# Optimization experiments

Measured on AMD Instinct MI355X. Metric: run time of the kernel, lower is better.

## Reference

```python
import jax, jax.numpy as jnp
import numpy as np

X_MIN, X_MAX = -3.0, 3.0
EPS = 1e-08


def setup_inputs() -> dict:
    key = jax.random.key(0)
    k1, k2, k3 = jax.random.split(key, 3)
    B, D_in, D_out, K = 8192, 512, 128, 16
    x = jax.random.normal(k1, (B, D_in), dtype=jnp.float32)
    # trunc_normal_(std=0.02) approximated by scaled normal
    weights = jax.random.normal(k2, (D_out, D_in, K), dtype=jnp.float32) * 0.02
    # xavier_uniform for skip
    limit = float(np.sqrt(6.0 / (D_in + D_out)))
    skip_w = jax.random.uniform(k3, (D_out, D_in), dtype=jnp.float32,
                                minval=-limit, maxval=limit)
    bias = jnp.zeros((D_out,), dtype=jnp.float32)
    return {"x": x, "weights": weights, "skip_w": skip_w, "bias": bias}


def reference(x, weights, skip_w, bias):
    # x: (B, D_in); weights: (D_out, D_in, K); skip_w: (D_out, D_in); bias: (D_out,)
    K = weights.shape[-1]
    t = jnp.clip((x - X_MIN) / (X_MAX - X_MIN + EPS), 0.0, 1.0)
    pos = t * (K - 1)
    idx0 = jnp.floor(pos).astype(jnp.int32)
    idx1 = jnp.minimum(idx0 + 1, K - 1)
    frac = jnp.clip(pos - idx0.astype(pos.dtype), 0.0, 1.0)
    # Hat-basis coefficients per (b, i): avoids materializing (B, D_out, D_in)
    oh0 = jax.nn.one_hot(idx0, K, dtype=x.dtype)  # (B, D_in, K)
    oh1 = jax.nn.one_hot(idx1, K, dtype=x.dtype)
    c = oh0 * (1.0 - frac)[..., None] + oh1 * frac[..., None]  # (B, D_in, K)
    # y[b,o] = sum_i (1-frac)*w[o,i,idx0] + frac*w[o,i,idx1]
    y = jnp.einsum('bik,oik->bo', c, weights)
    y = y + bias + x @ skip_w.T
    return y
```

## Files before the change

kernel.cpp:

```cpp
#include <hip/hip_runtime.h>

typedef _Float16 half8 __attribute__((ext_vector_type(8)));
typedef _Float16 h16 __attribute__((ext_vector_type(16)));
typedef float f32x4 __attribute__((ext_vector_type(4)));

#define DIN 512
#define DOUT 128
#define BTOT 8192
#define NCHUNK 68
#define NSPL 8
#define BM 128
#define CHUNK_BYTES 32768
#define CBASE 32768
#define LDS_BYTES 65536

__device__ static inline void llds16(const char* g, char* l) {
  __builtin_amdgcn_global_load_lds(
      (const __attribute__((address_space(1))) unsigned int*)g,
      (__attribute__((address_space(3))) unsigned int*)l, 16, 0, 0);
}

__device__ static inline unsigned short f2h(float x) {
  _Float16 h = (_Float16)x;
  return __builtin_bit_cast(unsigned short, h);
}

__global__ __launch_bounds__(256) void build_wpp(const float* __restrict__ w,
                                                 const float* __restrict__ sk,
                                                 unsigned short* __restrict__ wpp) {
  const int gid = blockIdx.x * 256 + threadIdx.x;
  const int g = gid >> 11;
  const int rem = gid & 2047;
  const int p = rem >> 7;
  const int o = rem & 127;
  const int kglob = g * 128 + p * 8;
  const float* src = (kglob < 8192) ? (w + (size_t)o * 8192 + kglob)
                                    : (sk + (size_t)o * 512 + (kglob - 8192));
  const float4 v0 = ((const float4*)src)[0];
  const float4 v1 = ((const float4*)src)[1];
  uint4 pk;
  pk.x = f2h(v0.x) | ((unsigned)f2h(v0.y) << 16);
  pk.y = f2h(v0.z) | ((unsigned)f2h(v0.w) << 16);
  pk.z = f2h(v1.x) | ((unsigned)f2h(v1.y) << 16);
  pk.w = f2h(v1.z) | ((unsigned)f2h(v1.w) << 16);
  ((uint4*)wpp)[gid] = pk;
}

__global__ __launch_bounds__(256) void xpose(const float* __restrict__ x,
                                             _Float16* __restrict__ xt) {
  __shared__ _Float16 t[32][33];
  const int c0 = blockIdx.x * 32;
  const int r0 = blockIdx.y * 32;
  const int tx = threadIdx.x & 31, ty = threadIdx.x >> 5;
#pragma unroll
  for (int j = 0; j < 32; j += 8)
    t[ty + j][tx] = (_Float16)x[(size_t)(r0 + ty + j) * DIN + c0 + tx];
  __syncthreads();
#pragma unroll
  for (int j = 0; j < 32; j += 8)
    xt[(size_t)(c0 + ty + j) * BTOT + r0 + tx] = t[tx][ty + j];
}

__global__ __launch_bounds__(256, 2) void kan_mfma(
    const float* __restrict__ x, const _Float16* __restrict__ xt,
    const unsigned short* __restrict__ wpp, const float* __restrict__ bias,
    float* __restrict__ out) {
  __shared__ __align__(16) char smem[LDS_BYTES];
  const int tid = threadIdx.x;
  const int bt = blockIdx.x >> 3;
  const int sp = blockIdx.x & 7;
  const int b0 = bt * BM;
  const int wid = tid >> 6, lane = tid & 63;
  const int lr = lane & 15, lq = lane >> 4;
  const int wm = wid & 1, wn = wid >> 1;

  const h16 iota16 = {(_Float16)0, (_Float16)1, (_Float16)2, (_Float16)3,
                      (_Float16)4, (_Float16)5, (_Float16)6, (_Float16)7,
                      (_Float16)8, (_Float16)9, (_Float16)10, (_Float16)11,
                      (_Float16)12, (_Float16)13, (_Float16)14, (_Float16)15};
  const h16 one16 = {(_Float16)1, (_Float16)1, (_Float16)1, (_Float16)1,
                     (_Float16)1, (_Float16)1, (_Float16)1, (_Float16)1,
                     (_Float16)1, (_Float16)1, (_Float16)1, (_Float16)1,
                     (_Float16)1, (_Float16)1, (_Float16)1, (_Float16)1};
  const h16 zero16 = {};

  f32x4 acc[4][4] = {};

  for (int c = 0; c < 9; ++c) {
    int g;
    bool skipc;
    if (c < 8) { g = sp + c * 8; skipc = false; }
    else { if (sp >= 4) break; g = 64 + sp; skipc = true; }

    __syncthreads();

    {
      const char* gsrc = (const char*)wpp + (size_t)g * CHUNK_BYTES + wid * 8192 + lane * 16;
      char* ldst = smem + wid * 8192;
#pragma unroll
      for (int it = 0; it < 8; ++it)
        llds16(gsrc + it * 1024, ldst + it * 1024);
    }

    if (!skipc) {
      const int ib = g * 8;
#pragma unroll
      for (int hh = 0; hh < 2; ++hh) {
        const int il = wid * 2 + hh;
#pragma unroll
        for (int rh = 0; rh < 2; ++rh) {
          const int r = lane + rh * 64;
          const float xv = (float)xt[(size_t)(ib + il) * BTOT + b0 + r];
          float t = fminf(fmaxf((xv + 3.0f) * (1.0f / 6.0f), 0.0f), 1.0f);
          const float pos = t * 15.0f;
          const _Float16 ph = (_Float16)pos;
          h16 pv;
#pragma unroll
          for (int q = 0; q < 16; ++q) pv[q] = ph;
          h16 d = __builtin_elementwise_abs(pv - iota16);
          h16 cc = __builtin_elementwise_max(one16 - d, zero16);
          char* base = smem + CBASE + (2 * il) * 2048 + r * 16;
          *(uint4*)base = ((const uint4*)&cc)[0];
          *(uint4*)(base + 2048) = ((const uint4*)&cc)[1];
        }
      }
    } else {
      const int ioff = (g - 64) * 128;
#pragma unroll
      for (int pp = 0; pp < 4; ++pp) {
        const int p = wid * 4 + pp;
#pragma unroll
        for (int rh = 0; rh < 2; ++rh) {
          const int r = lane + rh * 64;
          const float* src = x + (size_t)(b0 + r) * DIN + ioff + p * 8;
          const float4 v0 = ((const float4*)src)[0];
          const float4 v1 = ((const float4*)src)[1];
          uint4 pk;
          pk.x = f2h(v0.x) | ((unsigned)f2h(v0.y) << 16);
          pk.y = f2h(v0.z) | ((unsigned)f2h(v0.w) << 16);
          pk.z = f2h(v1.x) | ((unsigned)f2h(v1.y) << 16);
          pk.w = f2h(v1.z) | ((unsigned)f2h(v1.w) << 16);
          *(uint4*)(smem + CBASE + p * 2048 + r * 16) = pk;
        }
      }
    }
    __syncthreads();

#pragma unroll
    for (int ks = 0; ks < 4; ++ks) {
      const int slab = (ks * 4 + lq) * 2048 + lr * 16;
      half8 af[4], bf[4];
#pragma unroll
      for (int mt = 0; mt < 4; ++mt)
        af[mt] = *(const half8*)(smem + CBASE + slab + (wm * 64 + mt * 16) * 16);
#pragma unroll
      for (int nt = 0; nt < 4; ++nt)
        bf[nt] = *(const half8*)(smem + slab + (wn * 64 + nt * 16) * 16);
#pragma unroll
      for (int mt = 0; mt < 4; ++mt)
#pragma unroll
        for (int nt = 0; nt < 4; ++nt)
          acc[mt][nt] = __builtin_amdgcn_mfma_f32_16x16x32_f16(af[mt], bf[nt], acc[mt][nt], 0, 0, 0);
    }
  }

#pragma unroll
  for (int nt = 0; nt < 4; ++nt) {
    const int col = wn * 64 + nt * 16 + lr;
    const float bv = (sp == 0) ? bias[col] : 0.0f;
#pragma unroll
    for (int mt = 0; mt < 4; ++mt) {
      const int row0 = b0 + wm * 64 + mt * 16 + lq * 4;
#pragma unroll
      for (int r = 0; r < 4; ++r)
        atomicAdd(out + (size_t)(row0 + r) * DOUT + col, acc[mt][nt][r] + bv);
    }
  }
}

__global__ void kan_naive(const float* __restrict__ x, const float* __restrict__ w,
                          const float* __restrict__ skw, const float* __restrict__ bias,
                          float* __restrict__ out) {
  const int b = blockIdx.x;
  const int o = threadIdx.x;
  float acc = bias[o];
  for (int i = 0; i < DIN; ++i) {
    float xv = x[(size_t)b * DIN + i];
    float t = fminf(fmaxf((xv + 3.0f) * (1.0f / 6.0f), 0.0f), 1.0f);
    float p = t * 15.0f;
    float fi = floorf(p);
    int i0 = (int)fi;
    int i1 = (i0 < 15) ? i0 + 1 : 15;
    float f = p - fi;
    const float* wr = &w[((size_t)o * DIN + i) * 16];
    acc += (1.0f - f) * wr[i0] + f * wr[i1] + xv * skw[(size_t)o * DIN + i];
  }
  out[(size_t)b * DOUT + o] = acc;
}

extern "C" void kernel_launch(void* const* d_in, const int* in_sizes, int n_in,
                              void* d_out, int out_size, void* d_ws, size_t ws_size,
                              hipStream_t stream) {
  const float* x    = (const float*)d_in[0];
  const float* w    = (const float*)d_in[1];
  const float* skw  = (const float*)d_in[2];
  const float* bias = (const float*)d_in[3];
  float* out = (float*)d_out;

  const size_t xt_bytes = (size_t)DIN * BTOT * sizeof(_Float16);
  const size_t wpp_bytes = (size_t)NCHUNK * CHUNK_BYTES;
  if (ws_size < xt_bytes + wpp_bytes) {
    kan_naive<<<BTOT, DOUT, 0, stream>>>(x, w, skw, bias, out);
    return;
  }

  _Float16* xt = (_Float16*)d_ws;
  unsigned short* wpp = (unsigned short*)((char*)d_ws + xt_bytes);

  (void)hipMemsetAsync(d_out, 0, (size_t)out_size * sizeof(float), stream);
  build_wpp<<<NCHUNK * 2048 / 256, 256, 0, stream>>>(w, skw, wpp);
  xpose<<<dim3(DIN / 32, BTOT / 32), 256, 0, stream>>>(x, xt);
  kan_mfma<<<(BTOT / BM) * NSPL, 256, 0, stream>>>(x, xt, wpp, bias, out);
}
```

Baseline: 122.5 us.

## Read weight fragments from global memory directly and double the K-split

Weight B-fragments are now loaded directly from global/L2 into registers, so they are no longer staged into LDS with global_load_lds. This halves LDS per block, which allows a launch bound of 4 blocks per SM. The K-split goes from 8 to 16 so each block handles 4-5 chunks instead of 8-9, giving more blocks and more parallelism. The trade-offs are uncoalesced-ish global loads in the MFMA loop with no LDS reuse, and twice as many atomicAdds onto the output.

```diff
diff --git a/kernel.cpp b/kernel.cpp
--- a/kernel.cpp
+++ b/kernel.cpp
@@ -8,17 +8,10 @@
 #define DOUT 128
 #define BTOT 8192
 #define NCHUNK 68
-#define NSPL 8
+#define NSPL 16
 #define BM 128
 #define CHUNK_BYTES 32768
-#define CBASE 32768
-#define LDS_BYTES 65536
-
-__device__ static inline void llds16(const char* g, char* l) {
-  __builtin_amdgcn_global_load_lds(
-      (const __attribute__((address_space(1))) unsigned int*)g,
-      (__attribute__((address_space(3))) unsigned int*)l, 16, 0, 0);
-}
+#define LDS_BYTES 32768
 
 __device__ static inline unsigned short f2h(float x) {
   _Float16 h = (_Float16)x;
@@ -61,14 +54,14 @@
     xt[(size_t)(c0 + ty + j) * BTOT + r0 + tx] = t[tx][ty + j];
 }
 
-__global__ __launch_bounds__(256, 2) void kan_mfma(
+__global__ __launch_bounds__(256, 4) void kan_mfma(
     const float* __restrict__ x, const _Float16* __restrict__ xt,
     const unsigned short* __restrict__ wpp, const float* __restrict__ bias,
     float* __restrict__ out) {
   __shared__ __align__(16) char smem[LDS_BYTES];
   const int tid = threadIdx.x;
-  const int bt = blockIdx.x >> 3;
-  const int sp = blockIdx.x & 7;
+  const int bt = blockIdx.x >> 4;
+  const int sp = blockIdx.x & 15;
   const int b0 = bt * BM;
   const int wid = tid >> 6, lane = tid & 63;
   const int lr = lane & 15, lq = lane >> 4;
@@ -85,22 +78,13 @@
   const h16 zero16 = {};
 
   f32x4 acc[4][4] = {};
-
-  for (int c = 0; c < 9; ++c) {
-    int g;
-    bool skipc;
-    if (c < 8) { g = sp + c * 8; skipc = false; }
-    else { if (sp >= 4) break; g = 64 + sp; skipc = true; }
-
-    __syncthreads();
-
-    {
-      const char* gsrc = (const char*)wpp + (size_t)g * CHUNK_BYTES + wid * 8192 + lane * 16;
-      char* ldst = smem + wid * 8192;
-#pragma unroll
-      for (int it = 0; it < 8; ++it)
-        llds16(gsrc + it * 1024, ldst + it * 1024);
-    }
+  const int nch = (sp < 4) ? 5 : 4;
+
+  for (int j = 0; j < nch; ++j) {
+    const int g = (j < 4) ? (sp + j * 16) : (64 + sp);
+    const bool skipc = (j == 4);
+
+    if (j > 0) __syncthreads();
 
     if (!skipc) {
       const int ib = g * 8;
@@ -112,14 +96,13 @@
           const int r = lane + rh * 64;
           const float xv = (float)xt[(size_t)(ib + il) * BTOT + b0 + r];
           float t = fminf(fmaxf((xv + 3.0f) * (1.0f / 6.0f), 0.0f), 1.0f);
-          const float pos = t * 15.0f;
-          const _Float16 ph = (_Float16)pos;
+          const _Float16 ph = (_Float16)(t * 15.0f);
           h16 pv;
 #pragma unroll
           for (int q = 0; q < 16; ++q) pv[q] = ph;
           h16 d = __builtin_elementwise_abs(pv - iota16);
           h16 cc = __builtin_elementwise_max(one16 - d, zero16);
-          char* base = smem + CBASE + (2 * il) * 2048 + r * 16;
+          char* base = smem + (2 * il) * 2048 + r * 16;
           *(uint4*)base = ((const uint4*)&cc)[0];
           *(uint4*)(base + 2048) = ((const uint4*)&cc)[1];
         }
@@ -140,22 +123,24 @@
           pk.y = f2h(v0.z) | ((unsigned)f2h(v0.w) << 16);
           pk.z = f2h(v1.x) | ((unsigned)f2h(v1.y) << 16);
           pk.w = f2h(v1.z) | ((unsigned)f2h(v1.w) << 16);
-          *(uint4*)(smem + CBASE + p * 2048 + r * 16) = pk;
+          *(uint4*)(smem + p * 2048 + r * 16) = pk;
         }
       }
     }
     __syncthreads();
 
+    const char* wchunk = (const char*)wpp + (size_t)g * CHUNK_BYTES
+                       + (size_t)lq * 2048 + (size_t)(wn * 64 + lr) * 16;
 #pragma unroll
     for (int ks = 0; ks < 4; ++ks) {
       const int slab = (ks * 4 + lq) * 2048 + lr * 16;
       half8 af[4], bf[4];
 #pragma unroll
+      for (int nt = 0; nt < 4; ++nt)
+        bf[nt] = *(const half8*)(wchunk + ks * 8192 + nt * 256);
+#pragma unroll
       for (int mt = 0; mt < 4; ++mt)
-        af[mt] = *(const half8*)(smem + CBASE + slab + (wm * 64 + mt * 16) * 16);
-#pragma unroll
-      for (int nt = 0; nt < 4; ++nt)
-        bf[nt] = *(const half8*)(smem + slab + (wn * 64 + nt * 16) * 16);
+        af[mt] = *(const half8*)(smem + slab + (wm * 64 + mt * 16) * 16);
 #pragma unroll
       for (int mt = 0; mt < 4; ++mt)
 #pragma unroll
```

Measured after the change: 143.3 us. 1.17x slower.

## Generate hat coefficients in registers and switch to 32x32 MFMA with 17-way split

Applied to the files above, without the earlier changes.

Replaces the LDS-staged coefficient tile with hat-basis coefficients computed directly in registers, laid out as MFMA A fragments for 32x32x16 f16 instructions. The x transpose kernel becomes a plain row-major fp16 cast, and the skip-path A operands are read straight from global memory. The split-K factor goes from 8 to 17 (4 chunks per block), and halving LDS use allows 3 blocks per CU. In exchange there is more per-lane VALU work per MFMA, strided global reads of A, and more atomic adds into the output.

```diff
diff --git a/kernel.cpp b/kernel.cpp
--- a/kernel.cpp
+++ b/kernel.cpp
@@ -1,18 +1,16 @@
 #include <hip/hip_runtime.h>
 
 typedef _Float16 half8 __attribute__((ext_vector_type(8)));
-typedef _Float16 h16 __attribute__((ext_vector_type(16)));
-typedef float f32x4 __attribute__((ext_vector_type(4)));
+typedef float f32x16 __attribute__((ext_vector_type(16)));
 
 #define DIN 512
 #define DOUT 128
 #define BTOT 8192
 #define NCHUNK 68
-#define NSPL 8
+#define NSPL 17
 #define BM 128
 #define CHUNK_BYTES 32768
-#define CBASE 32768
-#define LDS_BYTES 65536
+#define LDS_BYTES 32768
 
 __device__ static inline void llds16(const char* g, char* l) {
   __builtin_amdgcn_global_load_lds(
@@ -46,54 +44,56 @@
   ((uint4*)wpp)[gid] = pk;
 }
 
-__global__ __launch_bounds__(256) void xpose(const float* __restrict__ x,
-                                             _Float16* __restrict__ xt) {
-  __shared__ _Float16 t[32][33];
-  const int c0 = blockIdx.x * 32;
-  const int r0 = blockIdx.y * 32;
-  const int tx = threadIdx.x & 31, ty = threadIdx.x >> 5;
-#pragma unroll
-  for (int j = 0; j < 32; j += 8)
-    t[ty + j][tx] = (_Float16)x[(size_t)(r0 + ty + j) * DIN + c0 + tx];
-  __syncthreads();
-#pragma unroll
-  for (int j = 0; j < 32; j += 8)
-    xt[(size_t)(c0 + ty + j) * BTOT + r0 + tx] = t[tx][ty + j];
-}
-
-__global__ __launch_bounds__(256, 2) void kan_mfma(
-    const float* __restrict__ x, const _Float16* __restrict__ xt,
-    const unsigned short* __restrict__ wpp, const float* __restrict__ bias,
-    float* __restrict__ out) {
+__global__ __launch_bounds__(256) void xcast(const float* __restrict__ x,
+                                             _Float16* __restrict__ xh) {
+  const int n = (blockIdx.x * 256 + threadIdx.x) * 4;
+  const float4 v = *(const float4*)(x + n);
+  unsigned lo = f2h(v.x) | ((unsigned)f2h(v.y) << 16);
+  unsigned hi = f2h(v.z) | ((unsigned)f2h(v.w) << 16);
+  *(uint2*)(xh + n) = make_uint2(lo, hi);
+}
+
+__global__ __launch_bounds__(256, 3) void kan_mfma(
+    const _Float16* __restrict__ xh, const unsigned short* __restrict__ wpp,
+    const float* __restrict__ bias, float* __restrict__ out) {
   __shared__ __align__(16) char smem[LDS_BYTES];
   const int tid = threadIdx.x;
-  const int bt = blockIdx.x >> 3;
-  const int sp = blockIdx.x & 7;
+  const unsigned u = blockIdx.x;
+  const int bt = u & 63;
+  const int sp = u >> 6;
   const int b0 = bt * BM;
   const int wid = tid >> 6, lane = tid & 63;
-  const int lr = lane & 15, lq = lane >> 4;
+  const int l5 = lane >> 5, l31 = lane & 31;
   const int wm = wid & 1, wn = wid >> 1;
 
-  const h16 iota16 = {(_Float16)0, (_Float16)1, (_Float16)2, (_Float16)3,
-                      (_Float16)4, (_Float16)5, (_Float16)6, (_Float16)7,
-                      (_Float16)8, (_Float16)9, (_Float16)10, (_Float16)11,
-                      (_Float16)12, (_Float16)13, (_Float16)14, (_Float16)15};
-  const h16 one16 = {(_Float16)1, (_Float16)1, (_Float16)1, (_Float16)1,
-                     (_Float16)1, (_Float16)1, (_Float16)1, (_Float16)1,
-                     (_Float16)1, (_Float16)1, (_Float16)1, (_Float16)1,
-                     (_Float16)1, (_Float16)1, (_Float16)1, (_Float16)1};
-  const h16 zero16 = {};
-
-  f32x4 acc[4][4] = {};
-
-  for (int c = 0; c < 9; ++c) {
-    int g;
-    bool skipc;
-    if (c < 8) { g = sp + c * 8; skipc = false; }
-    else { if (sp >= 4) break; g = 64 + sp; skipc = true; }
+  half8 iotaA, one8, three8, c6_8, fif8;
+  const half8 zero8 = {};
+#pragma unroll
+  for (int q = 0; q < 8; ++q) {
+    iotaA[q] = (_Float16)(l5 * 8 + q);
+    one8[q] = (_Float16)1.0f;
+    three8[q] = (_Float16)3.0f;
+    c6_8[q] = (_Float16)(1.0f / 6.0f);
+    fif8[q] = (_Float16)15.0f;
+  }
+
+  f32x16 acc[2][2] = {};
+
+#pragma unroll
+  for (int j = 0; j < 4; ++j) {
+    const int g = sp + j * 17;
+    const bool spl = (g < 64);
+
+    half8 asrc[2];
+    if (spl) {
+#pragma unroll
+      for (int mt = 0; mt < 2; ++mt) {
+        const int row = b0 + wm * 64 + mt * 32 + l31;
+        asrc[mt] = *(const half8*)(xh + (size_t)row * DIN + g * 8);
+      }
+    }
 
     __syncthreads();
-
     {
       const char* gsrc = (const char*)wpp + (size_t)g * CHUNK_BYTES + wid * 8192 + lane * 16;
       char* ldst = smem + wid * 8192;
@@ -101,79 +101,66 @@
       for (int it = 0; it < 8; ++it)
         llds16(gsrc + it * 1024, ldst + it * 1024);
     }
-
-    if (!skipc) {
-      const int ib = g * 8;
-#pragma unroll
-      for (int hh = 0; hh < 2; ++hh) {
-        const int il = wid * 2 + hh;
-#pragma unroll
-        for (int rh = 0; rh < 2; ++rh) {
-          const int r = lane + rh * 64;
-          const float xv = (float)xt[(size_t)(ib + il) * BTOT + b0 + r];
-          float t = fminf(fmaxf((xv + 3.0f) * (1.0f / 6.0f), 0.0f), 1.0f);
-          const float pos = t * 15.0f;
-          const _Float16 ph = (_Float16)pos;
-          h16 pv;
-#pragma unroll
-          for (int q = 0; q < 16; ++q) pv[q] = ph;
-          h16 d = __builtin_elementwise_abs(pv - iota16);
-          h16 cc = __builtin_elementwise_max(one16 - d, zero16);
-          char* base = smem + CBASE + (2 * il) * 2048 + r * 16;
-          *(uint4*)base = ((const uint4*)&cc)[0];
-          *(uint4*)(base + 2048) = ((const uint4*)&cc)[1];
+    __syncthreads();
+
+    if (spl) {
+      half8 pos[2];
+#pragma unroll
+      for (int mt = 0; mt < 2; ++mt) {
+        half8 a = (asrc[mt] + three8) * c6_8;
+        a = __builtin_elementwise_max(a, zero8);
+        a = __builtin_elementwise_min(a, one8);
+        pos[mt] = a * fif8;
+      }
+#pragma unroll
+      for (int kc = 0; kc < 8; ++kc) {
+        half8 bfr[2];
+#pragma unroll
+        for (int nt = 0; nt < 2; ++nt)
+          bfr[nt] = *(const half8*)(smem + (kc * 2 + l5) * 2048 + (wn * 64 + nt * 32 + l31) * 16);
+#pragma unroll
+        for (int mt = 0; mt < 2; ++mt) {
+          const _Float16 p = pos[mt][kc];
+          const half8 pv = {p, p, p, p, p, p, p, p};
+          const half8 d = __builtin_elementwise_abs(pv - iotaA);
+          const half8 cf = __builtin_elementwise_max(one8 - d, zero8);
+#pragma unroll
+          for (int nt = 0; nt < 2; ++nt)
+            acc[mt][nt] = __builtin_amdgcn_mfma_f32_32x32x16_f16(cf, bfr[nt], acc[mt][nt], 0, 0, 0);
         }
       }
     } else {
       const int ioff = (g - 64) * 128;
 #pragma unroll
-      for (int pp = 0; pp < 4; ++pp) {
-        const int p = wid * 4 + pp;
-#pragma unroll
-        for (int rh = 0; rh < 2; ++rh) {
-          const int r = lane + rh * 64;
-          const float* src = x + (size_t)(b0 + r) * DIN + ioff + p * 8;
-          const float4 v0 = ((const float4*)src)[0];
-          const float4 v1 = ((const float4*)src)[1];
-          uint4 pk;
-          pk.x = f2h(v0.x) | ((unsigned)f2h(v0.y) << 16);
-          pk.y = f2h(v0.z) | ((unsigned)f2h(v0.w) << 16);
-          pk.z = f2h(v1.x) | ((unsigned)f2h(v1.y) << 16);
-          pk.w = f2h(v1.z) | ((unsigned)f2h(v1.w) << 16);
-          *(uint4*)(smem + CBASE + p * 2048 + r * 16) = pk;
+      for (int kc = 0; kc < 8; ++kc) {
+        half8 bfr[2];
+#pragma unroll
+        for (int nt = 0; nt < 2; ++nt)
+          bfr[nt] = *(const half8*)(smem + (kc * 2 + l5) * 2048 + (wn * 64 + nt * 32 + l31) * 16);
+#pragma unroll
+        for (int mt = 0; mt < 2; ++mt) {
+          const int row = b0 + wm * 64 + mt * 32 + l31;
+          const half8 af = *(const half8*)(xh + (size_t)row * DIN + ioff + kc * 16 + l5 * 8);
+#pragma unroll
+          for (int nt = 0; nt < 2; ++nt)
+            acc[mt][nt] = __builtin_amdgcn_mfma_f32_32x32x16_f16(af, bfr[nt], acc[mt][nt], 0, 0, 0);
         }
       }
     }
-    __syncthreads();
-
-#pragma unroll
-    for (int ks = 0; ks < 4; ++ks) {
-      const int slab = (ks * 4 + lq) * 2048 + lr * 16;
-      half8 af[4], bf[4];
-#pragma unroll
-      for (int mt = 0; mt < 4; ++mt)
-        af[mt] = *(const half8*)(smem + CBASE + slab + (wm * 64 + mt * 16) * 16);
-#pragma unroll
-      for (int nt = 0; nt < 4; ++nt)
-        bf[nt] = *(const half8*)(smem + slab + (wn * 64 + nt * 16) * 16);
-#pragma unroll
-      for (int mt = 0; mt < 4; ++mt)
-#pragma unroll
-        for (int nt = 0; nt < 4; ++nt)
-          acc[mt][nt] = __builtin_amdgcn_mfma_f32_16x16x32_f16(af[mt], bf[nt], acc[mt][nt], 0, 0, 0);
-    }
-  }
-
-#pragma unroll
-  for (int nt = 0; nt < 4; ++nt) {
-    const int col = wn * 64 + nt * 16 + lr;
+  }
+
+#pragma unroll
+  for (int nt = 0; nt < 2; ++nt) {
+    const int col = wn * 64 + nt * 32 + l31;
     const float bv = (sp == 0) ? bias[col] : 0.0f;
 #pragma unroll
-    for (int mt = 0; mt < 4; ++mt) {
-      const int row0 = b0 + wm * 64 + mt * 16 + lq * 4;
-#pragma unroll
-      for (int r = 0; r < 4; ++r)
-        atomicAdd(out + (size_t)(row0 + r) * DOUT + col, acc[mt][nt][r] + bv);
+    for (int mt = 0; mt < 2; ++mt) {
+      const int rbase = b0 + wm * 64 + mt * 32 + 4 * l5;
+#pragma unroll
+      for (int r = 0; r < 16; ++r) {
+        const int row = rbase + (r & 3) + 8 * (r >> 2);
+        atomicAdd(out + (size_t)row * DOUT + col, acc[mt][nt][r] + bv);
+      }
     }
   }
 }
@@ -207,18 +194,18 @@
   const float* bias = (const float*)d_in[3];
   float* out = (float*)d_out;
 
-  const size_t xt_bytes = (size_t)DIN * BTOT * sizeof(_Float16);
+  const size_t xh_bytes = (size_t)BTOT * DIN * sizeof(_Float16);
   const size_t wpp_bytes = (size_t)NCHUNK * CHUNK_BYTES;
-  if (ws_size < xt_bytes + wpp_bytes) {
+  if (ws_size < xh_bytes + wpp_bytes) {
     kan_naive<<<BTOT, DOUT, 0, stream>>>(x, w, skw, bias, out);
     return;
   }
 
-  _Float16* xt = (_Float16*)d_ws;
-  unsigned short* wpp = (unsigned short*)((char*)d_ws + xt_bytes);
+  _Float16* xh = (_Float16*)d_ws;
+  unsigned short* wpp = (unsigned short*)((char*)d_ws + xh_bytes);
 
   (void)hipMemsetAsync(d_out, 0, (size_t)out_size * sizeof(float), stream);
   build_wpp<<<NCHUNK * 2048 / 256, 256, 0, stream>>>(w, skw, wpp);
-  xpose<<<dim3(DIN / 32, BTOT / 32), 256, 0, stream>>>(x, xt);
-  kan_mfma<<<(BTOT / BM) * NSPL, 256, 0, stream>>>(x, xt, wpp, bias, out);
-}
+  xcast<<<BTOT * DIN / 1024, 256, 0, stream>>>(x, xh);
+  kan_mfma<<<(BTOT / BM) * NSPL, 256, 0, stream>>>(xh, wpp, bias, out);
+}
```

Result: slower. 141.7 us (+15.7%).
